# Optimization experiments

Hardware: AMD Instinct MI355X
Metric: run time of the kernel (lower is better)

## Reference

```python
import jax, jax.numpy as jnp
import numpy as np

UP = jnp.array([0.0, 1.0, 0.0], dtype=jnp.float32)
LEASH = 15.0


def q_inv(q):
    return jnp.concatenate([-q[..., :3], q[..., 3:]], axis=-1)


def q_mul(q1, q2):
    x1, y1, z1, w1 = q1[..., 0], q1[..., 1], q1[..., 2], q1[..., 3]
    x2, y2, z2, w2 = q2[..., 0], q2[..., 1], q2[..., 2], q2[..., 3]
    return jnp.stack([
        w1 * x2 + x1 * w2 + y1 * z2 - z1 * y2,
        w1 * y2 - x1 * z2 + y1 * w2 + z1 * x2,
        w1 * z2 + x1 * y2 - y1 * x2 + z1 * w2,
        w1 * w2 - x1 * x2 - y1 * y2 - z1 * z2], axis=-1)


def q_rot(q, v):
    qv, qw = q[..., :3], q[..., 3:]
    t = 2.0 * jnp.cross(qv, v)
    return v + qw * t + jnp.cross(qv, t)


def mat_to_quat(R):
    # Batched [E,3,3] -> [E,4] (x,y,z,w), matching the torch branch structure.
    r = lambda i, j: R[:, i, j]
    eps = 1e-12
    tr = r(0, 0) + r(1, 1) + r(2, 2)
    Sa = jnp.sqrt(jnp.maximum(tr + 1.0, eps)) * 2.0
    qa = jnp.stack([(r(2, 1) - r(1, 2)) / Sa, (r(0, 2) - r(2, 0)) / Sa,
                    (r(1, 0) - r(0, 1)) / Sa, 0.25 * Sa], -1)
    Sb = jnp.sqrt(jnp.maximum(1.0 + r(0, 0) - r(1, 1) - r(2, 2), eps)) * 2.0
    qb = jnp.stack([0.25 * Sb, (r(0, 1) + r(1, 0)) / Sb,
                    (r(0, 2) + r(2, 0)) / Sb, (r(2, 1) - r(1, 2)) / Sb], -1)
    Sc = jnp.sqrt(jnp.maximum(1.0 + r(1, 1) - r(0, 0) - r(2, 2), eps)) * 2.0
    qc = jnp.stack([(r(0, 1) + r(1, 0)) / Sc, 0.25 * Sc,
                    (r(1, 2) + r(2, 1)) / Sc, (r(0, 2) - r(2, 0)) / Sc], -1)
    Sd = jnp.sqrt(jnp.maximum(1.0 + r(2, 2) - r(0, 0) - r(1, 1), eps)) * 2.0
    qd = jnp.stack([(r(0, 2) + r(2, 0)) / Sd, (r(1, 2) + r(2, 1)) / Sd,
                    0.25 * Sd, (r(1, 0) - r(0, 1)) / Sd], -1)
    cond_b = ((r(0, 0) > r(1, 1)) & (r(0, 0) > r(2, 2)))[:, None]
    cond_c = (r(1, 1) > r(2, 2))[:, None]
    return jnp.where((tr > 0)[:, None], qa,
                     jnp.where(cond_b, qb, jnp.where(cond_c, qc, qd)))


def sfm_pose_loss(pred_t, pred_q, gt_t, gt_q, batch_counts):
    E = batch_counts.shape[0]
    N = pred_t.shape[0]
    counts = batch_counts.astype(jnp.float32)  # [E]
    seg = jnp.repeat(jnp.arange(E), batch_counts, total_repeat_length=N)  # [N]
    starts = jnp.cumsum(batch_counts) - batch_counts  # first index of each episode
    sseg = lambda x: jax.ops.segment_sum(x, seg, num_segments=E)

    # --- per-episode centering ---
    mu_p = sseg(pred_t) / counts[:, None]
    mu_g = sseg(gt_t) / counts[:, None]
    p_c = pred_t - mu_p[seg]
    g_c = gt_t - mu_g[seg]

    # degenerate episodes: too short or near-zero gt variance (unbiased var)
    g_var = sseg(jnp.sum(g_c ** 2, -1)) / (counts - 1.0)
    deg = (batch_counts < 4) | (g_var < 1e-4)  # [E]

    # --- Umeyama: batched 3x3 SVD of H = p_c^T @ g_c per episode ---
    H = sseg(p_c[:, :, None] * g_c[:, None, :])  # [E,3,3]
    H_safe = jnp.where(deg[:, None, None], jnp.diag(jnp.array([3.0, 2.0, 1.0])), H)
    U, S, Vh = jnp.linalg.svd(H_safe, full_matrices=False)
    V = jnp.swapaxes(Vh, -1, -2)
    R0 = jnp.einsum('eij,ekj->eik', V, U)  # V @ U^T
    sgn = jnp.where(jnp.linalg.det(R0) < 0, -1.0, 1.0)
    V_adj = V * jnp.stack([jnp.ones_like(sgn), jnp.ones_like(sgn), sgn], -1)[:, None, :]
    R = jnp.einsum('eij,ekj->eik', V_adj, U)  # [E,3,3]

    p_rot = jnp.einsum('nij,nj->ni', R[seg], p_c)
    denom = sseg(jnp.sum(p_c ** 2, -1))
    nom = sseg(jnp.sum(p_rot * g_c, -1))
    s = jnp.where(denom > 1e-6,
                  jnp.clip(nom / jnp.maximum(denom, 1e-6), 1e-3, 1e3), 1.0)

    # --- translation loss (per-episode mse, then mean over episodes) ---
    p_al = jnp.where(deg[seg][:, None], p_c, p_rot * s[seg][:, None])
    diff = p_al - g_c
    loss_trans = jnp.mean(sseg(jnp.sum(diff ** 2, -1)) / (counts * 3.0))

    # --- scale loss (only non-degenerate episodes) ---
    loss_scale = jnp.sum(jnp.where(deg, 0.0, jnp.log(jnp.abs(s) + 1e-6) ** 2)) / E

    # --- rotation loss ---
    q_align = mat_to_quat(R)  # [E,4]
    q0_p = pred_q[starts]
    q0_g = gt_q[starts]
    pq_deg = q_mul(q_inv(q0_p)[seg], pred_q)
    gq_deg = q_mul(q_inv(q0_g)[seg], gt_q)
    pq_ume = q_mul(q_align[seg], pred_q)
    dm = deg[seg][:, None]
    pq_al = jnp.where(dm, pq_deg, pq_ume)
    gq_al = jnp.where(dm, gq_deg, gt_q)
    dot = jnp.sum(pq_al * gq_al, -1)
    loss_rot = jnp.mean(sseg(1.0 - dot ** 2) / counts)

    # --- gravity loss ---
    up = jnp.broadcast_to(UP, pred_q.shape[:-1] + (3,))
    pu = q_rot(q_inv(pred_q), up)
    gu = q_rot(q_inv(gt_q), up)
    cos = jnp.sum(pu * gu, -1) / jnp.maximum(
        jnp.linalg.norm(pu, axis=-1) * jnp.linalg.norm(gu, axis=-1), 1e-8)
    loss_grav = jnp.mean(sseg(1.0 - cos) / counts)

    # --- frame0 leash (deadzone on first translation of each episode) ---
    mag = jnp.linalg.norm(pred_t[starts], axis=-1)
    loss_leash = jnp.mean(jnp.maximum(mag - LEASH, 0.0) ** 2)

    return jnp.stack([loss_trans, loss_rot, loss_grav, loss_leash, loss_scale])


def setup_inputs() -> dict:
    rng = np.random.default_rng(0)
    E = 4096
    counts = rng.integers(64, 449, size=E)
    counts[:8] = np.array([2, 3, 3, 2, 3, 2, 3, 3])  # exercise degenerate branch
    N = int(counts.sum())
    key = jax.random.key(0)
    k1, k2, k3, k4 = jax.random.split(key, 4)
    pred_t = jax.random.normal(k1, (N, 3), dtype=jnp.float32) * 5.0
    gt_t = jax.random.normal(k2, (N, 3), dtype=jnp.float32) * 5.0

    def rand_unit_quat(k):
        q = jax.random.normal(k, (N, 4), dtype=jnp.float32)
        return q / jnp.linalg.norm(q, axis=-1, keepdims=True)

    return {
        'pred_t': pred_t,
        'pred_q': rand_unit_quat(k3),
        'gt_t': gt_t,
        'gt_q': rand_unit_quat(k4),
        'batch_counts': jnp.asarray(counts, dtype=jnp.int32),
    }


def reference(pred_t, pred_q, gt_t, gt_q, batch_counts):
    # Returns [loss_trans, loss_rot, loss_grav, loss_leash, loss_scale]
    return sfm_pose_loss(pred_t, pred_q, gt_t, gt_q, batch_counts)
```

## Files before the change

kernel.cpp:

```cpp
#include <hip/hip_runtime.h>
#include <math.h>

#define NACC 29

__device__ __forceinline__ float4 qmul4(float4 a, float4 b) {
    return make_float4(
        a.w*b.x + a.x*b.w + a.y*b.z - a.z*b.y,
        a.w*b.y - a.x*b.z + a.y*b.w + a.z*b.x,
        a.w*b.z + a.x*b.y - a.y*b.x + a.z*b.w,
        a.w*b.w - a.x*b.x - a.y*b.y - a.z*b.z);
}

__device__ __forceinline__ void qinv_rot_up(float4 q, float out[3]) {
    float qx = -q.x, qy = -q.y, qz = -q.z, qw = q.w;
    float tx = -2.f*qz;
    float ty = 0.f;
    float tz = 2.f*qx;
    out[0] = 0.f + qw*tx + (qy*tz - qz*ty);
    out[1] = 1.f + qw*ty + (qz*tx - qx*tz);
    out[2] = 0.f + qw*tz + (qx*ty - qy*tx);
}

__global__ void scan_zero_kernel(const int* __restrict__ counts,
                                 int* __restrict__ starts,
                                 float* __restrict__ out, int E) {
    __shared__ int lds[1024];
    int tid = threadIdx.x;
    if (tid < 5) out[tid] = 0.0f;
    int base = tid * 4;
    int c0 = (base + 0 < E) ? counts[base + 0] : 0;
    int c1 = (base + 1 < E) ? counts[base + 1] : 0;
    int c2 = (base + 2 < E) ? counts[base + 2] : 0;
    int c3 = (base + 3 < E) ? counts[base + 3] : 0;
    lds[tid] = c0 + c1 + c2 + c3;
    __syncthreads();
    for (int off = 1; off < 1024; off <<= 1) {
        int v = lds[tid];
        int a = (tid >= off) ? lds[tid - off] : 0;
        __syncthreads();
        lds[tid] = v + a;
        __syncthreads();
    }
    int excl = (tid > 0) ? lds[tid - 1] : 0;
    if (base + 0 < E) starts[base + 0] = excl; excl += c0;
    if (base + 1 < E) starts[base + 1] = excl; excl += c1;
    if (base + 2 < E) starts[base + 2] = excl; excl += c2;
    if (base + 3 < E) starts[base + 3] = excl;
}

__global__ __launch_bounds__(64) void pass1_kernel(
    const float* __restrict__ pred_t, const float4* __restrict__ pred_q,
    const float* __restrict__ gt_t,   const float4* __restrict__ gt_q,
    const int* __restrict__ counts, const int* __restrict__ starts,
    float* __restrict__ segacc)
{
    int e = blockIdx.x;
    int start = starts[e];
    int c = counts[e];
    float4 q0p = pred_q[start];
    float4 q0g = gt_q[start];
    float4 q0pi = make_float4(-q0p.x, -q0p.y, -q0p.z, q0p.w);
    float4 q0gi = make_float4(-q0g.x, -q0g.y, -q0g.z, q0g.w);

    float acc[NACC];
    #pragma unroll
    for (int k = 0; k < NACC; ++k) acc[k] = 0.f;

    for (int i = threadIdx.x; i < c; i += 64) {
        int n = start + i;
        float px = pred_t[3*n+0], py = pred_t[3*n+1], pz = pred_t[3*n+2];
        float gx = gt_t[3*n+0],  gy = gt_t[3*n+1],  gz = gt_t[3*n+2];
        float4 pq = pred_q[n];
        float4 gq = gt_q[n];

        acc[0] += px; acc[1] += py; acc[2] += pz;
        acc[3] += gx; acc[4] += gy; acc[5] += gz;
        acc[6] += px*px + py*py + pz*pz;
        acc[7] += gx*gx + gy*gy + gz*gz;
        acc[8]  += px*gx; acc[9]  += px*gy; acc[10] += px*gz;
        acc[11] += py*gx; acc[12] += py*gy; acc[13] += py*gz;
        acc[14] += pz*gx; acc[15] += pz*gy; acc[16] += pz*gz;

        float mx =  pq.w*gq.x - pq.z*gq.y + pq.y*gq.z - pq.x*gq.w;
        float my =  pq.z*gq.x + pq.w*gq.y - pq.x*gq.z - pq.y*gq.w;
        float mz = -pq.y*gq.x + pq.x*gq.y + pq.w*gq.z - pq.z*gq.w;
        float mw =  pq.x*gq.x + pq.y*gq.y + pq.z*gq.z + pq.w*gq.w;
        acc[17] += mx*mx; acc[18] += mx*my; acc[19] += mx*mz; acc[20] += mx*mw;
        acc[21] += my*my; acc[22] += my*mz; acc[23] += my*mw;
        acc[24] += mz*mz; acc[25] += mz*mw; acc[26] += mw*mw;

        float pu[3], gu[3];
        qinv_rot_up(pq, pu);
        qinv_rot_up(gq, gu);
        float nn = sqrtf(pu[0]*pu[0]+pu[1]*pu[1]+pu[2]*pu[2]) *
                   sqrtf(gu[0]*gu[0]+gu[1]*gu[1]+gu[2]*gu[2]);
        float cosv = (pu[0]*gu[0]+pu[1]*gu[1]+pu[2]*gu[2]) / fmaxf(nn, 1e-8f);
        acc[27] += 1.f - cosv;

        float4 aa = qmul4(q0pi, pq);
        float4 bb = qmul4(q0gi, gq);
        float dd = aa.x*bb.x + aa.y*bb.y + aa.z*bb.z + aa.w*bb.w;
        acc[28] += 1.f - dd*dd;
    }

    #pragma unroll
    for (int k = 0; k < NACC; ++k) {
        float v = acc[k];
        v += __shfl_xor(v, 32);
        v += __shfl_xor(v, 16);
        v += __shfl_xor(v, 8);
        v += __shfl_xor(v, 4);
        v += __shfl_xor(v, 2);
        v += __shfl_xor(v, 1);
        acc[k] = v;
    }
    float outv = 0.f;
    #pragma unroll
    for (int k = 0; k < NACC; ++k)
        if ((int)threadIdx.x == k) outv = acc[k];
    if (threadIdx.x < NACC)
        segacc[(size_t)e*32 + threadIdx.x] = outv;
}

__device__ void jacobi3f(float A[3][3], float V[3][3]) {
    V[0][0]=1.f; V[0][1]=0.f; V[0][2]=0.f;
    V[1][0]=0.f; V[1][1]=1.f; V[1][2]=0.f;
    V[2][0]=0.f; V[2][1]=0.f; V[2][2]=1.f;
    for (int sweep = 0; sweep < 6; ++sweep) {
        float off = A[0][1]*A[0][1] + A[0][2]*A[0][2] + A[1][2]*A[1][2];
        float dia = A[0][0]*A[0][0] + A[1][1]*A[1][1] + A[2][2]*A[2][2];
        if (off <= 1e-12f * (dia + 1e-30f)) break;
        for (int p = 0; p < 2; ++p) for (int q = p + 1; q < 3; ++q) {
            float apq = A[p][q];
            if (fabsf(apq) < 1e-30f) continue;
            float theta = (A[q][q] - A[p][p]) / (2.0f * apq);
            float t = ((theta >= 0.f) ? 1.f : -1.f) / (fabsf(theta) + sqrtf(theta*theta + 1.f));
            float cc = 1.f / sqrtf(t*t + 1.f);
            float ss = t * cc;
            float app = A[p][p], aqq = A[q][q];
            A[p][p] = app - t * apq;
            A[q][q] = aqq + t * apq;
            A[p][q] = 0.f; A[q][p] = 0.f;
            int r = 3 - p - q;
            float arp = A[r][p], arq = A[r][q];
            A[r][p] = cc*arp - ss*arq; A[p][r] = A[r][p];
            A[r][q] = ss*arp + cc*arq; A[q][r] = A[r][q];
            for (int i = 0; i < 3; ++i) {
                float vip = V[i][p], viq = V[i][q];
                V[i][p] = cc*vip - ss*viq;
                V[i][q] = ss*vip + cc*viq;
            }
        }
    }
}

__device__ void mat2quatf(const float R[3][3], float q[4]) {
    const float eps = 1e-12f;
    float tr = R[0][0] + R[1][1] + R[2][2];
    if (tr > 0.f) {
        float S = sqrtf(fmaxf(tr + 1.f, eps)) * 2.f;
        q[0] = (R[2][1]-R[1][2])/S; q[1] = (R[0][2]-R[2][0])/S;
        q[2] = (R[1][0]-R[0][1])/S; q[3] = 0.25f*S;
    } else if ((R[0][0] > R[1][1]) && (R[0][0] > R[2][2])) {
        float S = sqrtf(fmaxf(1.f + R[0][0] - R[1][1] - R[2][2], eps)) * 2.f;
        q[0] = 0.25f*S; q[1] = (R[0][1]+R[1][0])/S;
        q[2] = (R[0][2]+R[2][0])/S; q[3] = (R[2][1]-R[1][2])/S;
    } else if (R[1][1] > R[2][2]) {
        float S = sqrtf(fmaxf(1.f + R[1][1] - R[0][0] - R[2][2], eps)) * 2.f;
        q[0] = (R[0][1]+R[1][0])/S; q[1] = 0.25f*S;
        q[2] = (R[1][2]+R[2][1])/S; q[3] = (R[0][2]-R[2][0])/S;
    } else {
        float S = sqrtf(fmaxf(1.f + R[2][2] - R[0][0] - R[1][1], eps)) * 2.f;
        q[0] = (R[0][2]+R[2][0])/S; q[1] = (R[1][2]+R[2][1])/S;
        q[2] = 0.25f*S; q[3] = (R[1][0]-R[0][1])/S;
    }
}

__global__ __launch_bounds__(64) void finalize_kernel(
    const float* __restrict__ segacc, const int* __restrict__ counts,
    const int* __restrict__ starts, const float* __restrict__ pred_t,
    float* __restrict__ out, int E)
{
    int e = blockIdx.x * 64 + threadIdx.x;
    float v_trans = 0.f, v_rot = 0.f, v_grav = 0.f, v_leash = 0.f, v_scale = 0.f;
    if (e < E) {
        const float* A = segacc + (size_t)e * 32;
        int ci = counts[e];
        float c = (float)ci;
        float mu_p[3] = { A[0]/c, A[1]/c, A[2]/c };
        float mu_g[3] = { A[3]/c, A[4]/c, A[5]/c };
        float pp_c = A[6] - c*(mu_p[0]*mu_p[0]+mu_p[1]*mu_p[1]+mu_p[2]*mu_p[2]);
        float gg_c = A[7] - c*(mu_g[0]*mu_g[0]+mu_g[1]*mu_g[1]+mu_g[2]*mu_g[2]);
        float H[3][3];
        H[0][0]=A[8] -c*mu_p[0]*mu_g[0]; H[0][1]=A[9] -c*mu_p[0]*mu_g[1]; H[0][2]=A[10]-c*mu_p[0]*mu_g[2];
        H[1][0]=A[11]-c*mu_p[1]*mu_g[0]; H[1][1]=A[12]-c*mu_p[1]*mu_g[1]; H[1][2]=A[13]-c*mu_p[1]*mu_g[2];
        H[2][0]=A[14]-c*mu_p[2]*mu_g[0]; H[2][1]=A[15]-c*mu_p[2]*mu_g[1]; H[2][2]=A[16]-c*mu_p[2]*mu_g[2];
        float g_var = gg_c / (c - 1.0f);
        bool deg = (ci < 4) || (g_var < 1e-4f);
        float trH = H[0][0] + H[1][1] + H[2][2];
        float trans, rot, scale = 0.f;
        if (deg) {
            trans = (pp_c - 2.f*trH + gg_c) / (c * 3.f);
            rot = A[28] / c;
        } else {
            float B[3][3], V[3][3];
            for (int i = 0; i < 3; ++i)
                for (int j = 0; j < 3; ++j)
                    B[i][j] = H[0][i]*H[0][j] + H[1][i]*H[1][j] + H[2][i]*H[2][j];
            jacobi3f(B, V);
            float lam[3] = { B[0][0], B[1][1], B[2][2] };
            int idx[3] = {0, 1, 2};
            if (lam[idx[0]] < lam[idx[1]]) { int t = idx[0]; idx[0] = idx[1]; idx[1] = t; }
            if (lam[idx[0]] < lam[idx[2]]) { int t = idx[0]; idx[0] = idx[2]; idx[2] = t; }
            if (lam[idx[1]] < lam[idx[2]]) { int t = idx[1]; idx[1] = idx[2]; idx[2] = t; }
            float v1[3], v2[3], v3[3];
            for (int i = 0; i < 3; ++i) { v1[i] = V[i][idx[0]]; v2[i] = V[i][idx[1]]; v3[i] = V[i][idx[2]]; }
            float detV = v1[0]*(v2[1]*v3[2]-v2[2]*v3[1])
                       - v1[1]*(v2[0]*v3[2]-v2[2]*v3[0])
                       + v1[2]*(v2[0]*v3[1]-v2[1]*v3[0]);
            float sgnV = (detV < 0.f) ? -1.f : 1.f;
            float u1[3], u2[3], u3[3];
            for (int i = 0; i < 3; ++i) u1[i] = H[i][0]*v1[0] + H[i][1]*v1[1] + H[i][2]*v1[2];
            float n1 = sqrtf(u1[0]*u1[0]+u1[1]*u1[1]+u1[2]*u1[2]);
            n1 = fmaxf(n1, 1e-30f);
            for (int i = 0; i < 3; ++i) u1[i] /= n1;
            for (int i = 0; i < 3; ++i) u2[i] = H[i][0]*v2[0] + H[i][1]*v2[1] + H[i][2]*v2[2];
            float d12 = u1[0]*u2[0]+u1[1]*u2[1]+u1[2]*u2[2];
            for (int i = 0; i < 3; ++i) u2[i] -= d12*u1[i];
            float n2 = sqrtf(u2[0]*u2[0]+u2[1]*u2[1]+u2[2]*u2[2]);
            n2 = fmaxf(n2, 1e-30f);
            for (int i = 0; i < 3; ++i) u2[i] /= n2;
            u3[0] = u1[1]*u2[2] - u1[2]*u2[1];
            u3[1] = u1[2]*u2[0] - u1[0]*u2[2];
            u3[2] = u1[0]*u2[1] - u1[1]*u2[0];
            float R[3][3];
            for (int i = 0; i < 3; ++i)
                for (int k = 0; k < 3; ++k)
                    R[i][k] = v1[i]*u1[k] + v2[i]*u2[k] + sgnV*v3[i]*u3[k];
            float nom = 0.f;
            for (int k = 0; k < 3; ++k)
                for (int j = 0; j < 3; ++j)
                    nom += R[k][j] * H[j][k];
            float denom = pp_c;
            float s = 1.f;
            if (denom > 1e-6f) {
                s = nom / fmaxf(denom, 1e-6f);
                s = fminf(fmaxf(s, 1e-3f), 1e3f);
            }
            trans = (s*s*denom - 2.f*s*nom + gg_c) / (c * 3.f);
            float ls = logf(fabsf(s) + 1e-6f);
            scale = ls * ls;
            float q[4];
            mat2quatf(R, q);
            float M00=A[17], M01=A[18], M02=A[19], M03=A[20], M11=A[21],
                  M12=A[22], M13=A[23], M22=A[24], M23=A[25], M33=A[26];
            float quad = q[0]*q[0]*M00 + q[1]*q[1]*M11 + q[2]*q[2]*M22 + q[3]*q[3]*M33
                + 2.f*(q[0]*q[1]*M01 + q[0]*q[2]*M02 + q[0]*q[3]*M03
                     + q[1]*q[2]*M12 + q[1]*q[3]*M13 + q[2]*q[3]*M23);
            rot = (c - quad) / c;
        }
        float grav = A[27] / c;
        int st = starts[e];
        float tx = pred_t[3*st+0], ty = pred_t[3*st+1], tz = pred_t[3*st+2];
        float mag = sqrtf(tx*tx + ty*ty + tz*tz);
        float ml = fmaxf(mag - 15.f, 0.f);
        float Ed = (float)E;
        v_trans = trans / Ed;
        v_rot   = rot / Ed;
        v_grav  = grav / Ed;
        v_leash = (ml * ml) / Ed;
        v_scale = scale / Ed;
    }
    float vals[5] = { v_trans, v_rot, v_grav, v_leash, v_scale };
    #pragma unroll
    for (int k = 0; k < 5; ++k) {
        float v = vals[k];
        v += __shfl_down(v, 32);
        v += __shfl_down(v, 16);
        v += __shfl_down(v, 8);
        v += __shfl_down(v, 4);
        v += __shfl_down(v, 2);
        v += __shfl_down(v, 1);
        if (threadIdx.x == 0) atomicAdd(out + k, v);
    }
}

extern "C" void kernel_launch(void* const* d_in, const int* in_sizes, int n_in,
                              void* d_out, int out_size, void* d_ws, size_t ws_size,
                              hipStream_t stream) {
    const float*  pred_t = (const float*)d_in[0];
    const float4* pred_q = (const float4*)d_in[1];
    const float*  gt_t   = (const float*)d_in[2];
    const float4* gt_q   = (const float4*)d_in[3];
    const int*    counts = (const int*)d_in[4];
    int E = in_sizes[4];

    int* starts = (int*)d_ws;
    size_t off = ((size_t)E * sizeof(int) + 255) & ~(size_t)255;
    float* segacc = (float*)((char*)d_ws + off);

    scan_zero_kernel<<<1, 1024, 0, stream>>>(counts, starts, (float*)d_out, E);
    pass1_kernel<<<E, 64, 0, stream>>>(pred_t, pred_q, gt_t, gt_q, counts, starts, segacc);
    finalize_kernel<<<(E + 63) / 64, 64, 0, stream>>>(segacc, counts, starts, pred_t,
                                                      (float*)d_out, E);
}
```

Measured before the change: 121.8 us.

## Fuse per-episode accumulation and finalize into one wave-per-episode kernel

Merges the accumulation pass and the finalize kernel into a single kernel in which each 64-lane wave owns one episode, computes the 3x3 SVD/Procrustes step redundantly across lanes, and atomically adds the per-episode losses. This removes one launch and the segacc round trip through global memory. The degenerate-branch quaternion term is now computed only for small episodes, with a rare second pass when the variance test triggers. Blocks are grown to 4 waves. In exchange it adds 5 atomics per episode (20k total) and runs the serial Jacobi on every lane of the wave.

```diff
diff --git a/kernel.cpp b/kernel.cpp
--- a/kernel.cpp
+++ b/kernel.cpp
@@ -1,25 +1,5 @@
 #include <hip/hip_runtime.h>
 #include <math.h>
-
-#define NACC 29
-
-__device__ __forceinline__ float4 qmul4(float4 a, float4 b) {
-    return make_float4(
-        a.w*b.x + a.x*b.w + a.y*b.z - a.z*b.y,
-        a.w*b.y - a.x*b.z + a.y*b.w + a.z*b.x,
-        a.w*b.z + a.x*b.y - a.y*b.x + a.z*b.w,
-        a.w*b.w - a.x*b.x - a.y*b.y - a.z*b.z);
-}
-
-__device__ __forceinline__ void qinv_rot_up(float4 q, float out[3]) {
-    float qx = -q.x, qy = -q.y, qz = -q.z, qw = q.w;
-    float tx = -2.f*qz;
-    float ty = 0.f;
-    float tz = 2.f*qx;
-    out[0] = 0.f + qw*tx + (qy*tz - qz*ty);
-    out[1] = 1.f + qw*ty + (qz*tx - qx*tz);
-    out[2] = 0.f + qw*tz + (qx*ty - qy*tx);
-}
 
 __global__ void scan_zero_kernel(const int* __restrict__ counts,
                                  int* __restrict__ starts,
@@ -48,78 +28,32 @@
     if (base + 3 < E) starts[base + 3] = excl;
 }
 
-__global__ __launch_bounds__(64) void pass1_kernel(
-    const float* __restrict__ pred_t, const float4* __restrict__ pred_q,
-    const float* __restrict__ gt_t,   const float4* __restrict__ gt_q,
-    const int* __restrict__ counts, const int* __restrict__ starts,
-    float* __restrict__ segacc)
-{
-    int e = blockIdx.x;
-    int start = starts[e];
-    int c = counts[e];
-    float4 q0p = pred_q[start];
-    float4 q0g = gt_q[start];
-    float4 q0pi = make_float4(-q0p.x, -q0p.y, -q0p.z, q0p.w);
-    float4 q0gi = make_float4(-q0g.x, -q0g.y, -q0g.z, q0g.w);
-
-    float acc[NACC];
-    #pragma unroll
-    for (int k = 0; k < NACC; ++k) acc[k] = 0.f;
-
-    for (int i = threadIdx.x; i < c; i += 64) {
-        int n = start + i;
-        float px = pred_t[3*n+0], py = pred_t[3*n+1], pz = pred_t[3*n+2];
-        float gx = gt_t[3*n+0],  gy = gt_t[3*n+1],  gz = gt_t[3*n+2];
-        float4 pq = pred_q[n];
-        float4 gq = gt_q[n];
-
-        acc[0] += px; acc[1] += py; acc[2] += pz;
-        acc[3] += gx; acc[4] += gy; acc[5] += gz;
-        acc[6] += px*px + py*py + pz*pz;
-        acc[7] += gx*gx + gy*gy + gz*gz;
-        acc[8]  += px*gx; acc[9]  += px*gy; acc[10] += px*gz;
-        acc[11] += py*gx; acc[12] += py*gy; acc[13] += py*gz;
-        acc[14] += pz*gx; acc[15] += pz*gy; acc[16] += pz*gz;
-
-        float mx =  pq.w*gq.x - pq.z*gq.y + pq.y*gq.z - pq.x*gq.w;
-        float my =  pq.z*gq.x + pq.w*gq.y - pq.x*gq.z - pq.y*gq.w;
-        float mz = -pq.y*gq.x + pq.x*gq.y + pq.w*gq.z - pq.z*gq.w;
-        float mw =  pq.x*gq.x + pq.y*gq.y + pq.z*gq.z + pq.w*gq.w;
-        acc[17] += mx*mx; acc[18] += mx*my; acc[19] += mx*mz; acc[20] += mx*mw;
-        acc[21] += my*my; acc[22] += my*mz; acc[23] += my*mw;
-        acc[24] += mz*mz; acc[25] += mz*mw; acc[26] += mw*mw;
-
-        float pu[3], gu[3];
-        qinv_rot_up(pq, pu);
-        qinv_rot_up(gq, gu);
-        float nn = sqrtf(pu[0]*pu[0]+pu[1]*pu[1]+pu[2]*pu[2]) *
-                   sqrtf(gu[0]*gu[0]+gu[1]*gu[1]+gu[2]*gu[2]);
-        float cosv = (pu[0]*gu[0]+pu[1]*gu[1]+pu[2]*gu[2]) / fmaxf(nn, 1e-8f);
-        acc[27] += 1.f - cosv;
-
-        float4 aa = qmul4(q0pi, pq);
-        float4 bb = qmul4(q0gi, gq);
-        float dd = aa.x*bb.x + aa.y*bb.y + aa.z*bb.z + aa.w*bb.w;
-        acc[28] += 1.f - dd*dd;
-    }
-
-    #pragma unroll
-    for (int k = 0; k < NACC; ++k) {
-        float v = acc[k];
-        v += __shfl_xor(v, 32);
-        v += __shfl_xor(v, 16);
-        v += __shfl_xor(v, 8);
-        v += __shfl_xor(v, 4);
-        v += __shfl_xor(v, 2);
-        v += __shfl_xor(v, 1);
-        acc[k] = v;
-    }
-    float outv = 0.f;
-    #pragma unroll
-    for (int k = 0; k < NACC; ++k)
-        if ((int)threadIdx.x == k) outv = acc[k];
-    if (threadIdx.x < NACC)
-        segacc[(size_t)e*32 + threadIdx.x] = outv;
+__device__ __forceinline__ float4 qmul4(float4 a, float4 b) {
+    return make_float4(
+        a.w*b.x + a.x*b.w + a.y*b.z - a.z*b.y,
+        a.w*b.y - a.x*b.z + a.y*b.w + a.z*b.x,
+        a.w*b.z + a.x*b.y - a.y*b.x + a.z*b.w,
+        a.w*b.w - a.x*b.x - a.y*b.y - a.z*b.z);
+}
+
+__device__ __forceinline__ void qinv_rot_up(float4 q, float out[3]) {
+    float qx = -q.x, qy = -q.y, qz = -q.z, qw = q.w;
+    float tx = -2.f*qz;
+    float ty = 0.f;
+    float tz = 2.f*qx;
+    out[0] = 0.f + qw*tx + (qy*tz - qz*ty);
+    out[1] = 1.f + qw*ty + (qz*tx - qx*tz);
+    out[2] = 0.f + qw*tz + (qx*ty - qy*tx);
+}
+
+__device__ __forceinline__ float wave_sum(float v) {
+    v += __shfl_xor(v, 32);
+    v += __shfl_xor(v, 16);
+    v += __shfl_xor(v, 8);
+    v += __shfl_xor(v, 4);
+    v += __shfl_xor(v, 2);
+    v += __shfl_xor(v, 1);
+    return v;
 }
 
 __device__ void jacobi3f(float A[3][3], float V[3][3]) {
@@ -176,112 +110,165 @@
     }
 }
 
-__global__ __launch_bounds__(64) void finalize_kernel(
-    const float* __restrict__ segacc, const int* __restrict__ counts,
-    const int* __restrict__ starts, const float* __restrict__ pred_t,
+__global__ __launch_bounds__(256) void fused_kernel(
+    const float* __restrict__ pred_t, const float4* __restrict__ pred_q,
+    const float* __restrict__ gt_t,   const float4* __restrict__ gt_q,
+    const int* __restrict__ counts, const int* __restrict__ starts,
     float* __restrict__ out, int E)
 {
-    int e = blockIdx.x * 64 + threadIdx.x;
-    float v_trans = 0.f, v_rot = 0.f, v_grav = 0.f, v_leash = 0.f, v_scale = 0.f;
-    if (e < E) {
-        const float* A = segacc + (size_t)e * 32;
-        int ci = counts[e];
-        float c = (float)ci;
-        float mu_p[3] = { A[0]/c, A[1]/c, A[2]/c };
-        float mu_g[3] = { A[3]/c, A[4]/c, A[5]/c };
-        float pp_c = A[6] - c*(mu_p[0]*mu_p[0]+mu_p[1]*mu_p[1]+mu_p[2]*mu_p[2]);
-        float gg_c = A[7] - c*(mu_g[0]*mu_g[0]+mu_g[1]*mu_g[1]+mu_g[2]*mu_g[2]);
-        float H[3][3];
-        H[0][0]=A[8] -c*mu_p[0]*mu_g[0]; H[0][1]=A[9] -c*mu_p[0]*mu_g[1]; H[0][2]=A[10]-c*mu_p[0]*mu_g[2];
-        H[1][0]=A[11]-c*mu_p[1]*mu_g[0]; H[1][1]=A[12]-c*mu_p[1]*mu_g[1]; H[1][2]=A[13]-c*mu_p[1]*mu_g[2];
-        H[2][0]=A[14]-c*mu_p[2]*mu_g[0]; H[2][1]=A[15]-c*mu_p[2]*mu_g[1]; H[2][2]=A[16]-c*mu_p[2]*mu_g[2];
-        float g_var = gg_c / (c - 1.0f);
-        bool deg = (ci < 4) || (g_var < 1e-4f);
+    int wv = threadIdx.x >> 6;
+    int lane = threadIdx.x & 63;
+    int e = blockIdx.x * 4 + wv;
+    if (e >= E) return;
+    int start = starts[e];
+    int ci = counts[e];
+    float4 q0p = pred_q[start];
+    float4 q0g = gt_q[start];
+    float4 q0pi = make_float4(-q0p.x, -q0p.y, -q0p.z, q0p.w);
+    float4 q0gi = make_float4(-q0g.x, -q0g.y, -q0g.z, q0g.w);
+    float t0x = pred_t[3*start+0], t0y = pred_t[3*start+1], t0z = pred_t[3*start+2];
+    bool small_c = (ci < 4);
+
+    float acc[28];
+    #pragma unroll
+    for (int k = 0; k < 28; ++k) acc[k] = 0.f;
+    float acc28 = 0.f;
+
+    for (int i = lane; i < ci; i += 64) {
+        int n = start + i;
+        float px = pred_t[3*n+0], py = pred_t[3*n+1], pz = pred_t[3*n+2];
+        float gx = gt_t[3*n+0],  gy = gt_t[3*n+1],  gz = gt_t[3*n+2];
+        float4 pq = pred_q[n];
+        float4 gq = gt_q[n];
+
+        acc[0] += px; acc[1] += py; acc[2] += pz;
+        acc[3] += gx; acc[4] += gy; acc[5] += gz;
+        acc[6] += px*px + py*py + pz*pz;
+        acc[7] += gx*gx + gy*gy + gz*gz;
+        acc[8]  += px*gx; acc[9]  += px*gy; acc[10] += px*gz;
+        acc[11] += py*gx; acc[12] += py*gy; acc[13] += py*gz;
+        acc[14] += pz*gx; acc[15] += pz*gy; acc[16] += pz*gz;
+
+        float mx =  pq.w*gq.x - pq.z*gq.y + pq.y*gq.z - pq.x*gq.w;
+        float my =  pq.z*gq.x + pq.w*gq.y - pq.x*gq.z - pq.y*gq.w;
+        float mz = -pq.y*gq.x + pq.x*gq.y + pq.w*gq.z - pq.z*gq.w;
+        float mw =  pq.x*gq.x + pq.y*gq.y + pq.z*gq.z + pq.w*gq.w;
+        acc[17] += mx*mx; acc[18] += mx*my; acc[19] += mx*mz; acc[20] += mx*mw;
+        acc[21] += my*my; acc[22] += my*mz; acc[23] += my*mw;
+        acc[24] += mz*mz; acc[25] += mz*mw; acc[26] += mw*mw;
+
+        float pu[3], gu[3];
+        qinv_rot_up(pq, pu);
+        qinv_rot_up(gq, gu);
+        float nn = sqrtf(pu[0]*pu[0]+pu[1]*pu[1]+pu[2]*pu[2]) *
+                   sqrtf(gu[0]*gu[0]+gu[1]*gu[1]+gu[2]*gu[2]);
+        float cosv = (pu[0]*gu[0]+pu[1]*gu[1]+pu[2]*gu[2]) / fmaxf(nn, 1e-8f);
+        acc[27] += 1.f - cosv;
+
+        if (small_c) {
+            float4 aa = qmul4(q0pi, pq);
+            float4 bb = qmul4(q0gi, gq);
+            float dd = aa.x*bb.x + aa.y*bb.y + aa.z*bb.z + aa.w*bb.w;
+            acc28 += 1.f - dd*dd;
+        }
+    }
+
+    #pragma unroll
+    for (int k = 0; k < 28; ++k) acc[k] = wave_sum(acc[k]);
+
+    float c = (float)ci;
+    float mu_p[3] = { acc[0]/c, acc[1]/c, acc[2]/c };
+    float mu_g[3] = { acc[3]/c, acc[4]/c, acc[5]/c };
+    float pp_c = acc[6] - c*(mu_p[0]*mu_p[0]+mu_p[1]*mu_p[1]+mu_p[2]*mu_p[2]);
+    float gg_c = acc[7] - c*(mu_g[0]*mu_g[0]+mu_g[1]*mu_g[1]+mu_g[2]*mu_g[2]);
+    float H[3][3];
+    H[0][0]=acc[8] -c*mu_p[0]*mu_g[0]; H[0][1]=acc[9] -c*mu_p[0]*mu_g[1]; H[0][2]=acc[10]-c*mu_p[0]*mu_g[2];
+    H[1][0]=acc[11]-c*mu_p[1]*mu_g[0]; H[1][1]=acc[12]-c*mu_p[1]*mu_g[1]; H[1][2]=acc[13]-c*mu_p[1]*mu_g[2];
+    H[2][0]=acc[14]-c*mu_p[2]*mu_g[0]; H[2][1]=acc[15]-c*mu_p[2]*mu_g[1]; H[2][2]=acc[16]-c*mu_p[2]*mu_g[2];
+    float g_var = gg_c / (c - 1.0f);
+    bool deg = small_c || (g_var < 1e-4f);
+    float trans, rot, scale = 0.f;
+    if (deg) {
+        float s28;
+        if (small_c) {
+            s28 = wave_sum(acc28);
+        } else {
+            float local = 0.f;
+            for (int i = lane; i < ci; i += 64) {
+                int n = start + i;
+                float4 aa = qmul4(q0pi, pred_q[n]);
+                float4 bb = qmul4(q0gi, gt_q[n]);
+                float dd = aa.x*bb.x + aa.y*bb.y + aa.z*bb.z + aa.w*bb.w;
+                local += 1.f - dd*dd;
+            }
+            s28 = wave_sum(local);
+        }
         float trH = H[0][0] + H[1][1] + H[2][2];
-        float trans, rot, scale = 0.f;
-        if (deg) {
-            trans = (pp_c - 2.f*trH + gg_c) / (c * 3.f);
-            rot = A[28] / c;
-        } else {
-            float B[3][3], V[3][3];
-            for (int i = 0; i < 3; ++i)
-                for (int j = 0; j < 3; ++j)
-                    B[i][j] = H[0][i]*H[0][j] + H[1][i]*H[1][j] + H[2][i]*H[2][j];
-            jacobi3f(B, V);
-            float lam[3] = { B[0][0], B[1][1], B[2][2] };
-            int idx[3] = {0, 1, 2};
-            if (lam[idx[0]] < lam[idx[1]]) { int t = idx[0]; idx[0] = idx[1]; idx[1] = t; }
-            if (lam[idx[0]] < lam[idx[2]]) { int t = idx[0]; idx[0] = idx[2]; idx[2] = t; }
-            if (lam[idx[1]] < lam[idx[2]]) { int t = idx[1]; idx[1] = idx[2]; idx[2] = t; }
-            float v1[3], v2[3], v3[3];
-            for (int i = 0; i < 3; ++i) { v1[i] = V[i][idx[0]]; v2[i] = V[i][idx[1]]; v3[i] = V[i][idx[2]]; }
-            float detV = v1[0]*(v2[1]*v3[2]-v2[2]*v3[1])
-                       - v1[1]*(v2[0]*v3[2]-v2[2]*v3[0])
-                       + v1[2]*(v2[0]*v3[1]-v2[1]*v3[0]);
-            float sgnV = (detV < 0.f) ? -1.f : 1.f;
-            float u1[3], u2[3], u3[3];
-            for (int i = 0; i < 3; ++i) u1[i] = H[i][0]*v1[0] + H[i][1]*v1[1] + H[i][2]*v1[2];
-            float n1 = sqrtf(u1[0]*u1[0]+u1[1]*u1[1]+u1[2]*u1[2]);
-            n1 = fmaxf(n1, 1e-30f);
-            for (int i = 0; i < 3; ++i) u1[i] /= n1;
-            for (int i = 0; i < 3; ++i) u2[i] = H[i][0]*v2[0] + H[i][1]*v2[1] + H[i][2]*v2[2];
-            float d12 = u1[0]*u2[0]+u1[1]*u2[1]+u1[2]*u2[2];
-            for (int i = 0; i < 3; ++i) u2[i] -= d12*u1[i];
-            float n2 = sqrtf(u2[0]*u2[0]+u2[1]*u2[1]+u2[2]*u2[2]);
-            n2 = fmaxf(n2, 1e-30f);
-            for (int i = 0; i < 3; ++i) u2[i] /= n2;
-            u3[0] = u1[1]*u2[2] - u1[2]*u2[1];
-            u3[1] = u1[2]*u2[0] - u1[0]*u2[2];
-            u3[2] = u1[0]*u2[1] - u1[1]*u2[0];
-            float R[3][3];
-            for (int i = 0; i < 3; ++i)
-                for (int k = 0; k < 3; ++k)
-                    R[i][k] = v1[i]*u1[k] + v2[i]*u2[k] + sgnV*v3[i]*u3[k];
-            float nom = 0.f;
+        trans = (pp_c - 2.f*trH + gg_c) / (c * 3.f);
+        rot = s28 / c;
+    } else {
+        float B[3][3], V[3][3];
+        for (int i = 0; i < 3; ++i)
+            for (int j = 0; j < 3; ++j)
+                B[i][j] = H[0][i]*H[0][j] + H[1][i]*H[1][j] + H[2][i]*H[2][j];
+        jacobi3f(B, V);
+        float lam[3] = { B[0][0], B[1][1], B[2][2] };
+        int idx[3] = {0, 1, 2};
+        if (lam[idx[0]] < lam[idx[1]]) { int t = idx[0]; idx[0] = idx[1]; idx[1] = t; }
+        if (lam[idx[0]] < lam[idx[2]]) { int t = idx[0]; idx[0] = idx[2]; idx[2] = t; }
+        if (lam[idx[1]] < lam[idx[2]]) { int t = idx[1]; idx[1] = idx[2]; idx[2] = t; }
+        float v1[3], v2[3], v3[3];
+        for (int i = 0; i < 3; ++i) { v1[i] = V[i][idx[0]]; v2[i] = V[i][idx[1]]; v3[i] = V[i][idx[2]]; }
+        float detV = v1[0]*(v2[1]*v3[2]-v2[2]*v3[1])
+                   - v1[1]*(v2[0]*v3[2]-v2[2]*v3[0])
+                   + v1[2]*(v2[0]*v3[1]-v2[1]*v3[0]);
+        float sgnV = (detV < 0.f) ? -1.f : 1.f;
+        float u1[3], u2[3], u3[3];
+        for (int i = 0; i < 3; ++i) u1[i] = H[i][0]*v1[0] + H[i][1]*v1[1] + H[i][2]*v1[2];
+        float n1 = fmaxf(sqrtf(u1[0]*u1[0]+u1[1]*u1[1]+u1[2]*u1[2]), 1e-30f);
+        for (int i = 0; i < 3; ++i) u1[i] /= n1;
+        for (int i = 0; i < 3; ++i) u2[i] = H[i][0]*v2[0] + H[i][1]*v2[1] + H[i][2]*v2[2];
+        float d12 = u1[0]*u2[0]+u1[1]*u2[1]+u1[2]*u2[2];
+        for (int i = 0; i < 3; ++i) u2[i] -= d12*u1[i];
+        float n2 = fmaxf(sqrtf(u2[0]*u2[0]+u2[1]*u2[1]+u2[2]*u2[2]), 1e-30f);
+        for (int i = 0; i < 3; ++i) u2[i] /= n2;
+        u3[0] = u1[1]*u2[2] - u1[2]*u2[1];
+        u3[1] = u1[2]*u2[0] - u1[0]*u2[2];
+        u3[2] = u1[0]*u2[1] - u1[1]*u2[0];
+        float R[3][3];
+        for (int i = 0; i < 3; ++i)
             for (int k = 0; k < 3; ++k)
-                for (int j = 0; j < 3; ++j)
-                    nom += R[k][j] * H[j][k];
-            float denom = pp_c;
-            float s = 1.f;
-            if (denom > 1e-6f) {
-                s = nom / fmaxf(denom, 1e-6f);
-                s = fminf(fmaxf(s, 1e-3f), 1e3f);
-            }
-            trans = (s*s*denom - 2.f*s*nom + gg_c) / (c * 3.f);
-            float ls = logf(fabsf(s) + 1e-6f);
-            scale = ls * ls;
-            float q[4];
-            mat2quatf(R, q);
-            float M00=A[17], M01=A[18], M02=A[19], M03=A[20], M11=A[21],
-                  M12=A[22], M13=A[23], M22=A[24], M23=A[25], M33=A[26];
-            float quad = q[0]*q[0]*M00 + q[1]*q[1]*M11 + q[2]*q[2]*M22 + q[3]*q[3]*M33
-                + 2.f*(q[0]*q[1]*M01 + q[0]*q[2]*M02 + q[0]*q[3]*M03
-                     + q[1]*q[2]*M12 + q[1]*q[3]*M13 + q[2]*q[3]*M23);
-            rot = (c - quad) / c;
-        }
-        float grav = A[27] / c;
-        int st = starts[e];
-        float tx = pred_t[3*st+0], ty = pred_t[3*st+1], tz = pred_t[3*st+2];
-        float mag = sqrtf(tx*tx + ty*ty + tz*tz);
+                R[i][k] = v1[i]*u1[k] + v2[i]*u2[k] + sgnV*v3[i]*u3[k];
+        float nom = 0.f;
+        for (int k = 0; k < 3; ++k)
+            for (int j = 0; j < 3; ++j)
+                nom += R[k][j] * H[j][k];
+        float denom = pp_c;
+        float s = 1.f;
+        if (denom > 1e-6f) {
+            s = nom / fmaxf(denom, 1e-6f);
+            s = fminf(fmaxf(s, 1e-3f), 1e3f);
+        }
+        trans = (s*s*denom - 2.f*s*nom + gg_c) / (c * 3.f);
+        float ls = logf(fabsf(s) + 1e-6f);
+        scale = ls * ls;
+        float q[4];
+        mat2quatf(R, q);
+        float quad = q[0]*q[0]*acc[17] + q[1]*q[1]*acc[21] + q[2]*q[2]*acc[24] + q[3]*q[3]*acc[26]
+            + 2.f*(q[0]*q[1]*acc[18] + q[0]*q[2]*acc[19] + q[0]*q[3]*acc[20]
+                 + q[1]*q[2]*acc[22] + q[1]*q[3]*acc[23] + q[2]*q[3]*acc[25]);
+        rot = (c - quad) / c;
+    }
+    if (lane == 0) {
+        float grav = acc[27] / c;
+        float mag = sqrtf(t0x*t0x + t0y*t0y + t0z*t0z);
         float ml = fmaxf(mag - 15.f, 0.f);
         float Ed = (float)E;
-        v_trans = trans / Ed;
-        v_rot   = rot / Ed;
-        v_grav  = grav / Ed;
-        v_leash = (ml * ml) / Ed;
-        v_scale = scale / Ed;
-    }
-    float vals[5] = { v_trans, v_rot, v_grav, v_leash, v_scale };
-    #pragma unroll
-    for (int k = 0; k < 5; ++k) {
-        float v = vals[k];
-        v += __shfl_down(v, 32);
-        v += __shfl_down(v, 16);
-        v += __shfl_down(v, 8);
-        v += __shfl_down(v, 4);
-        v += __shfl_down(v, 2);
-        v += __shfl_down(v, 1);
-        if (threadIdx.x == 0) atomicAdd(out + k, v);
+        atomicAdd(out + 0, trans / Ed);
+        atomicAdd(out + 1, rot / Ed);
+        atomicAdd(out + 2, grav / Ed);
+        atomicAdd(out + 3, (ml * ml) / Ed);
+        atomicAdd(out + 4, scale / Ed);
     }
 }
 
@@ -296,11 +283,8 @@
     int E = in_sizes[4];
 
     int* starts = (int*)d_ws;
-    size_t off = ((size_t)E * sizeof(int) + 255) & ~(size_t)255;
-    float* segacc = (float*)((char*)d_ws + off);
 
     scan_zero_kernel<<<1, 1024, 0, stream>>>(counts, starts, (float*)d_out, E);
-    pass1_kernel<<<E, 64, 0, stream>>>(pred_t, pred_q, gt_t, gt_q, counts, starts, segacc);
-    finalize_kernel<<<(E + 63) / 64, 64, 0, stream>>>(segacc, counts, starts, pred_t,
-                                                      (float*)d_out, E);
-}
+    fused_kernel<<<(E + 3) / 4, 256, 0, stream>>>(pred_t, pred_q, gt_t, gt_q,
+                                                  counts, starts, (float*)d_out, E);
+}
```

Result: slower. 359.1 us (+195.0%).
